# Kernel optimization log

Hardware: AMD Instinct MI355X
Metric: run time of the kernel (lower is better)

## Reference

```python
import jax, jax.numpy as jnp
import numpy as np

FACTOR = 1.0   # module's self.factor
EPS = 1e-6     # rmsnorm eps


def setup_inputs() -> dict:
    key = jax.random.key(0)
    k0, k1, k2, k3 = jax.random.split(key, 4)
    B, S = 4, 2048
    D_IN = D_STATE = D_OUT = 2048
    N_HEADS = 32
    HD = D_STATE // N_HEADS  # 64
    x = jax.random.normal(k0, (B, S, D_IN), jnp.float32)
    w_in = jax.random.normal(k1, (D_STATE, D_IN), jnp.float32) * 0.02
    b_in = jnp.zeros((D_STATE,), jnp.float32)
    state_weight = jax.random.normal(k2, (N_HEADS, HD, HD), jnp.float32) * 0.02
    norm_weight = jnp.ones((D_STATE,), jnp.float32)
    w_out = jax.random.normal(k3, (D_OUT, D_STATE), jnp.float32) * (0.02 / np.sqrt(2 * 24))
    return dict(x=x, w_in=w_in, b_in=b_in, state_weight=state_weight,
                norm_weight=norm_weight, w_out=w_out)


def _rnn_scan(xt, W):
    # xt: (B, S, N, H); W: (N, H, H)
    B, S, N, H = xt.shape

    def step(s, x_t):
        # s: (B, N, H) ; per-head linear recurrence with tanh nonlinearity
        s = jnp.tanh(jnp.einsum('bnh,nhk->bnk', s, W) + x_t)
        return s, s

    s0 = jnp.zeros((B, N, H), xt.dtype)
    _, states = jax.lax.scan(step, s0, jnp.swapaxes(xt, 0, 1))  # (S, B, N, H)
    return jnp.swapaxes(states, 0, 1)  # (B, S, N, H)


def reference(x, w_in, b_in, state_weight, norm_weight, w_out):
    B, S, _ = x.shape
    N, H, _ = state_weight.shape
    h = x @ w_in.T + b_in                      # input_projection: (B,S,state)
    h = h.reshape(B, S, N, H) * FACTOR
    W = state_weight * FACTOR
    states = _rnn_scan(h, W)                   # (B,S,N,H)
    y = states.reshape(B, S, N * H)
    # rmsnorm
    y = y * jax.lax.rsqrt(jnp.mean(y * y, axis=-1, keepdims=True) + EPS) * norm_weight
    return y @ w_out.T                         # output_projection (no bias)
```

## Files before the change

kernel.cpp:

```cpp
#include <hip/hip_runtime.h>
#include <hip/hip_bf16.h>
#include <cstdint>


typedef short bf16x8 __attribute__((ext_vector_type(8)));
typedef float f32x4 __attribute__((ext_vector_type(4)));
typedef _Float16 f16x2 __attribute__((ext_vector_type(2)));

#define GLD16(gp, lp)                                                          \
  __builtin_amdgcn_global_load_lds(                                            \
      (const __attribute__((address_space(1))) void*)(gp),                     \
      (__attribute__((address_space(3))) void*)(lp), 16, 0, 0)

__global__ __launch_bounds__(256) void cvt_f32_bf16(
    const float* __restrict__ in, __hip_bfloat16* __restrict__ out, int n4) {
  int i = blockIdx.x * 256 + threadIdx.x;
  if (i >= n4) return;
  float4 v = ((const float4*)in)[i];
  __hip_bfloat16 a = __float2bfloat16(v.x);
  __hip_bfloat16 b = __float2bfloat16(v.y);
  __hip_bfloat16 c = __float2bfloat16(v.z);
  __hip_bfloat16 d = __float2bfloat16(v.w);
  ushort4 p;
  p.x = *(unsigned short*)&a; p.y = *(unsigned short*)&b;
  p.z = *(unsigned short*)&c; p.w = *(unsigned short*)&d;
  ((ushort4*)out)[i] = p;
}

__global__ __launch_bounds__(512) void gemm_nt(
    const __hip_bfloat16* __restrict__ A, const __hip_bfloat16* __restrict__ B,
    const float* __restrict__ bias, float* __restrict__ C,
    int M, int N, int K) {
  __shared__ __hip_bfloat16 As[2][256 * 32];
  __shared__ __hip_bfloat16 Bs[2][256 * 32];
  const int tid  = threadIdx.x;
  const int lane = tid & 63;
  const int wave = tid >> 6;
  const int wm = wave >> 2;
  const int wn = wave & 3;

  const int id = blockIdx.y * gridDim.x + blockIdx.x;
  const int v = (id & 7) * 32 + (id >> 3);
  const long bm = (long)(v >> 3) * 256;
  const long bn = (long)(v & 7) * 256;

  const int r0 = tid >> 2;
  const int k0 = (tid & 3) * 8;
  const __hip_bfloat16* gA0 = A + (bm + r0) * (long)K + k0;
  const __hip_bfloat16* gA1 = A + (bm + 128 + r0) * (long)K + k0;
  const __hip_bfloat16* gB0 = B + (bn + r0) * (long)K + k0;
  const __hip_bfloat16* gB1 = B + (bn + 128 + r0) * (long)K + k0;

#define STAGE(sbuf, kt)                                                        \
  do {                                                                         \
    GLD16(gA0 + (kt) * 32, &As[sbuf][wave * 512]);                             \
    GLD16(gA1 + (kt) * 32, &As[sbuf][4096 + wave * 512]);                      \
    GLD16(gB0 + (kt) * 32, &Bs[sbuf][wave * 512]);                             \
    GLD16(gB1 + (kt) * 32, &Bs[sbuf][4096 + wave * 512]);                      \
  } while (0)

  const int fr = lane & 15;
  const int fk = (lane >> 4) * 8;

  f32x4 acc[8][4];
#pragma unroll
  for (int i = 0; i < 8; i++)
#pragma unroll
    for (int j = 0; j < 4; j++) acc[i][j] = {0.f, 0.f, 0.f, 0.f};

  STAGE(0, 0);

  const int nk = K >> 5;
  for (int kt = 0; kt < nk; kt++) {
    const int cur = kt & 1;
    if (kt + 1 < nk) {
      STAGE(cur ^ 1, kt + 1);
      asm volatile("s_waitcnt vmcnt(4)" ::: "memory");
    } else {
      asm volatile("s_waitcnt vmcnt(0)" ::: "memory");
    }
    __builtin_amdgcn_s_barrier();
    __builtin_amdgcn_sched_barrier(0);
    bf16x8 af[8], bfr[4];
#pragma unroll
    for (int t = 0; t < 8; t++)
      af[t] = *(const bf16x8*)&As[cur][(wm * 128 + t * 16 + fr) * 32 + fk];
#pragma unroll
    for (int t = 0; t < 4; t++)
      bfr[t] = *(const bf16x8*)&Bs[cur][(wn * 64 + t * 16 + fr) * 32 + fk];
    __builtin_amdgcn_s_setprio(1);
#pragma unroll
    for (int i = 0; i < 8; i++)
#pragma unroll
      for (int j = 0; j < 4; j++)
        acc[i][j] = __builtin_amdgcn_mfma_f32_16x16x32_bf16(
            af[i], bfr[j], acc[i][j], 0, 0, 0);
    __builtin_amdgcn_s_setprio(0);
    __builtin_amdgcn_sched_barrier(0);
    __builtin_amdgcn_s_barrier();
  }
#undef STAGE

  const int cr = (lane >> 4) * 4;
  const int cc = lane & 15;
#pragma unroll
  for (int j = 0; j < 4; j++) {
    const long n = bn + wn * 64 + j * 16 + cc;
    const float bv = bias ? bias[n] : 0.0f;
#pragma unroll
    for (int i = 0; i < 8; i++) {
      const long m = bm + wm * 128 + i * 16 + cr;
#pragma unroll
      for (int r = 0; r < 4; r++)
        C[(m + r) * (long)N + n] = acc[i][j][r] + bv;
    }
  }
}

__device__ __forceinline__ float tanh_fast(float z) {
  float e = __builtin_amdgcn_exp2f(z * 2.8853900817779268f);
  return 1.0f - 2.0f * __builtin_amdgcn_rcpf(e + 1.0f);
}

__global__ __launch_bounds__(64) void scan_kernel(
    const float* __restrict__ Wst, float* __restrict__ h) {
  const int b = blockIdx.x >> 5;
  const int n = blockIdx.x & 31;
  const int lane = threadIdx.x;
  const float* Wn = Wst + n * 4096;

  f16x2 w2[32];
#pragma unroll
  for (int p = 0; p < 32; p++) {
    f16x2 t;
    t.x = (_Float16)Wn[(2 * p) * 64 + lane];
    t.y = (_Float16)Wn[(2 * p + 1) * 64 + lane];
    w2[p] = t;
  }

  __shared__ alignas(16) unsigned short s_h[64];

  int4 sv[8];
#pragma unroll
  for (int q = 0; q < 8; q++) sv[q] = make_int4(0, 0, 0, 0);

  float* hp = h + ((size_t)b * 2048) * 2048 + n * 64 + lane;
  float xcur[8], xnxt[8];
#pragma unroll
  for (int i = 0; i < 8; i++) xcur[i] = hp[(size_t)i * 2048];

  const f16x2 z2 = {(_Float16)0.f, (_Float16)0.f};

  for (int t0 = 0; t0 < 2048; t0 += 8) {
    if (t0 + 8 < 2048) {
#pragma unroll
      for (int i = 0; i < 8; i++)
        xnxt[i] = hp[(size_t)(t0 + 8 + i) * 2048];
    }
#pragma unroll
    for (int i = 0; i < 8; i++) {
      f16x2 ac0 = z2, ac1 = z2, ac2 = z2, ac3 = z2;
#pragma unroll
      for (int q = 0; q < 8; q++) {
        ac0 = __builtin_elementwise_fma(__builtin_bit_cast(f16x2, sv[q].x),
                                        w2[4 * q + 0], ac0);
        ac1 = __builtin_elementwise_fma(__builtin_bit_cast(f16x2, sv[q].y),
                                        w2[4 * q + 1], ac1);
        ac2 = __builtin_elementwise_fma(__builtin_bit_cast(f16x2, sv[q].z),
                                        w2[4 * q + 2], ac2);
        ac3 = __builtin_elementwise_fma(__builtin_bit_cast(f16x2, sv[q].w),
                                        w2[4 * q + 3], ac3);
      }
      f16x2 p01 = ac0 + ac1;
      f16x2 p23 = ac2 + ac3;
      f16x2 pt = p01 + p23;
      float z = (float)pt.x + (float)pt.y + xcur[i];
      float sn = tanh_fast(z);
      _Float16 sh = (_Float16)sn;
      s_h[lane] = __builtin_bit_cast(unsigned short, sh);
#pragma unroll
      for (int q = 0; q < 8; q++) sv[q] = ((const int4*)s_h)[q];
      hp[(size_t)(t0 + i) * 2048] = sn;
    }
#pragma unroll
    for (int i = 0; i < 8; i++) xcur[i] = xnxt[i];
  }
}

__global__ __launch_bounds__(256) void rmsnorm_to_bf16(
    const float* __restrict__ Y, const float* __restrict__ g,
    __hip_bfloat16* __restrict__ O) {
  const long row = blockIdx.x;
  const float* yr = Y + row * 2048;
  const int tid = threadIdx.x;
  float4 v0 = ((const float4*)yr)[tid * 2];
  float4 v1 = ((const float4*)yr)[tid * 2 + 1];
  float ss = v0.x * v0.x + v0.y * v0.y + v0.z * v0.z + v0.w * v0.w +
             v1.x * v1.x + v1.y * v1.y + v1.z * v1.z + v1.w * v1.w;
#pragma unroll
  for (int off = 32; off > 0; off >>= 1) ss += __shfl_down(ss, off);
  __shared__ float red[4];
  if ((tid & 63) == 0) red[tid >> 6] = ss;
  __syncthreads();
  float inv = rsqrtf((red[0] + red[1] + red[2] + red[3]) * (1.0f / 2048.0f)
                     + 1e-6f);
  float4 g0 = ((const float4*)(g + tid * 8))[0];
  float4 g1 = ((const float4*)(g + tid * 8))[1];
  float ov[8] = {v0.x * inv * g0.x, v0.y * inv * g0.y,
                 v0.z * inv * g0.z, v0.w * inv * g0.w,
                 v1.x * inv * g1.x, v1.y * inv * g1.y,
                 v1.z * inv * g1.z, v1.w * inv * g1.w};
  ushort4 p0, p1;
  __hip_bfloat16 t;
  t = __float2bfloat16(ov[0]); p0.x = *(unsigned short*)&t;
  t = __float2bfloat16(ov[1]); p0.y = *(unsigned short*)&t;
  t = __float2bfloat16(ov[2]); p0.z = *(unsigned short*)&t;
  t = __float2bfloat16(ov[3]); p0.w = *(unsigned short*)&t;
  t = __float2bfloat16(ov[4]); p1.x = *(unsigned short*)&t;
  t = __float2bfloat16(ov[5]); p1.y = *(unsigned short*)&t;
  t = __float2bfloat16(ov[6]); p1.z = *(unsigned short*)&t;
  t = __float2bfloat16(ov[7]); p1.w = *(unsigned short*)&t;
  ushort4* op = (ushort4*)(O + row * 2048 + tid * 8);
  op[0] = p0;
  op[1] = p1;
}

extern "C" void kernel_launch(void* const* d_in, const int* in_sizes, int n_in,
                              void* d_out, int out_size, void* d_ws,
                              size_t ws_size, hipStream_t stream) {
  const float* x     = (const float*)d_in[0];
  const float* w_in  = (const float*)d_in[1];
  const float* b_in  = (const float*)d_in[2];
  const float* w_st  = (const float*)d_in[3];
  const float* nw    = (const float*)d_in[4];
  const float* w_out = (const float*)d_in[5];
  float* out = (float*)d_out;

  char* ws = (char*)d_ws;
  __hip_bfloat16* x_bf  = (__hip_bfloat16*)(ws);
  __hip_bfloat16* wi_bf = (__hip_bfloat16*)(ws + 33554432);
  __hip_bfloat16* wo_bf = (__hip_bfloat16*)(ws + 41943040);
  float* h              = (float*)(ws + 50331648);

  cvt_f32_bf16<<<16384, 256, 0, stream>>>(x, x_bf, 4194304);
  cvt_f32_bf16<<<4096, 256, 0, stream>>>(w_in, wi_bf, 1048576);
  cvt_f32_bf16<<<4096, 256, 0, stream>>>(w_out, wo_bf, 1048576);

  gemm_nt<<<dim3(8, 32), 512, 0, stream>>>(x_bf, wi_bf, b_in, h,
                                           8192, 2048, 2048);
  scan_kernel<<<128, 64, 0, stream>>>(w_st, h);
  rmsnorm_to_bf16<<<8192, 256, 0, stream>>>(h, nw, x_bf);
  gemm_nt<<<dim3(8, 32), 512, 0, stream>>>(x_bf, wo_bf, nullptr, out,
                                           8192, 2048, 2048);
}
```

Baseline: 710.4 us.

## Double K-tile depth to 64 with XOR-swizzled LDS layout in GEMM

Raises the GEMM K step from 32 to 64 per iteration, halving the number of barrier-synchronised loop trips and issuing twice as many MFMAs between barriers. LDS rows are now 64 bf16 wide, with an XOR swizzle on the 16-byte column chunk to avoid bank conflicts on fragment reads. This doubles LDS use to 128 KB per block and raises register pressure from the doubled fragments. The launch bound of two blocks per CU may not be reachable with that much shared memory.

```diff
diff --git a/kernel.cpp b/kernel.cpp
--- a/kernel.cpp
+++ b/kernel.cpp
@@ -27,12 +27,12 @@
   ((ushort4*)out)[i] = p;
 }
 
-__global__ __launch_bounds__(512) void gemm_nt(
+__global__ __launch_bounds__(512, 2) void gemm_nt(
     const __hip_bfloat16* __restrict__ A, const __hip_bfloat16* __restrict__ B,
     const float* __restrict__ bias, float* __restrict__ C,
     int M, int N, int K) {
-  __shared__ __hip_bfloat16 As[2][256 * 32];
-  __shared__ __hip_bfloat16 Bs[2][256 * 32];
+  __shared__ __hip_bfloat16 As[2][256 * 64];
+  __shared__ __hip_bfloat16 Bs[2][256 * 64];
   const int tid  = threadIdx.x;
   const int lane = tid & 63;
   const int wave = tid >> 6;
@@ -44,23 +44,30 @@
   const long bm = (long)(v >> 3) * 256;
   const long bn = (long)(v & 7) * 256;
 
-  const int r0 = tid >> 2;
-  const int k0 = (tid & 3) * 8;
-  const __hip_bfloat16* gA0 = A + (bm + r0) * (long)K + k0;
-  const __hip_bfloat16* gA1 = A + (bm + 128 + r0) * (long)K + k0;
-  const __hip_bfloat16* gB0 = B + (bn + r0) * (long)K + k0;
-  const __hip_bfloat16* gB1 = B + (bn + 128 + r0) * (long)K + k0;
+  const int srow = (wave << 3) + (lane >> 3);
+  const int scol = (((lane & 7) ^ ((lane >> 3) & 7)) << 3);
+  const __hip_bfloat16* gA = A + (bm + srow) * (long)K + scol;
+  const __hip_bfloat16* gB = B + (bn + srow) * (long)K + scol;
+  const long rstep = 64 * (long)K;
 
 #define STAGE(sbuf, kt)                                                        \
   do {                                                                         \
-    GLD16(gA0 + (kt) * 32, &As[sbuf][wave * 512]);                             \
-    GLD16(gA1 + (kt) * 32, &As[sbuf][4096 + wave * 512]);                      \
-    GLD16(gB0 + (kt) * 32, &Bs[sbuf][wave * 512]);                             \
-    GLD16(gB1 + (kt) * 32, &Bs[sbuf][4096 + wave * 512]);                      \
+    const long ko_ = (long)(kt) * 64;                                          \
+    GLD16(gA + ko_,             &As[sbuf][wave * 512]);                        \
+    GLD16(gA + ko_ + rstep,     &As[sbuf][4096 + wave * 512]);                 \
+    GLD16(gA + ko_ + 2 * rstep, &As[sbuf][8192 + wave * 512]);                 \
+    GLD16(gA + ko_ + 3 * rstep, &As[sbuf][12288 + wave * 512]);                \
+    GLD16(gB + ko_,             &Bs[sbuf][wave * 512]);                        \
+    GLD16(gB + ko_ + rstep,     &Bs[sbuf][4096 + wave * 512]);                 \
+    GLD16(gB + ko_ + 2 * rstep, &Bs[sbuf][8192 + wave * 512]);                 \
+    GLD16(gB + ko_ + 3 * rstep, &Bs[sbuf][12288 + wave * 512]);                \
   } while (0)
 
-  const int fr = lane & 15;
-  const int fk = (lane >> 4) * 8;
+  const int fr  = lane & 15;
+  const int fk8 = (lane >> 4) * 8;
+  const int xr  = (fr & 7) << 3;
+  const int ac0 = fk8 ^ xr;
+  const int ac1 = (32 + fk8) ^ xr;
 
   f32x4 acc[8][4];
 #pragma unroll
@@ -69,32 +76,43 @@
     for (int j = 0; j < 4; j++) acc[i][j] = {0.f, 0.f, 0.f, 0.f};
 
   STAGE(0, 0);
-
-  const int nk = K >> 5;
+  asm volatile("s_waitcnt vmcnt(0)" ::: "memory");
+  __builtin_amdgcn_s_barrier();
+
+  const int nk = K >> 6;
   for (int kt = 0; kt < nk; kt++) {
     const int cur = kt & 1;
     if (kt + 1 < nk) {
       STAGE(cur ^ 1, kt + 1);
-      asm volatile("s_waitcnt vmcnt(4)" ::: "memory");
+      asm volatile("s_waitcnt vmcnt(8)" ::: "memory");
     } else {
       asm volatile("s_waitcnt vmcnt(0)" ::: "memory");
     }
     __builtin_amdgcn_s_barrier();
     __builtin_amdgcn_sched_barrier(0);
-    bf16x8 af[8], bfr[4];
-#pragma unroll
-    for (int t = 0; t < 8; t++)
-      af[t] = *(const bf16x8*)&As[cur][(wm * 128 + t * 16 + fr) * 32 + fk];
-#pragma unroll
-    for (int t = 0; t < 4; t++)
-      bfr[t] = *(const bf16x8*)&Bs[cur][(wn * 64 + t * 16 + fr) * 32 + fk];
+    bf16x8 af[8][2], bfr[4][2];
+#pragma unroll
+    for (int t = 0; t < 8; t++) {
+      const int rb = (wm * 128 + t * 16 + fr) * 64;
+      af[t][0] = *(const bf16x8*)&As[cur][rb + ac0];
+      af[t][1] = *(const bf16x8*)&As[cur][rb + ac1];
+    }
+#pragma unroll
+    for (int j = 0; j < 4; j++) {
+      const int rb = (wn * 64 + j * 16 + fr) * 64;
+      bfr[j][0] = *(const bf16x8*)&Bs[cur][rb + ac0];
+      bfr[j][1] = *(const bf16x8*)&Bs[cur][rb + ac1];
+    }
     __builtin_amdgcn_s_setprio(1);
 #pragma unroll
     for (int i = 0; i < 8; i++)
 #pragma unroll
-      for (int j = 0; j < 4; j++)
+      for (int j = 0; j < 4; j++) {
         acc[i][j] = __builtin_amdgcn_mfma_f32_16x16x32_bf16(
-            af[i], bfr[j], acc[i][j], 0, 0, 0);
+            af[i][0], bfr[j][0], acc[i][j], 0, 0, 0);
+        acc[i][j] = __builtin_amdgcn_mfma_f32_16x16x32_bf16(
+            af[i][1], bfr[j][1], acc[i][j], 0, 0, 0);
+      }
     __builtin_amdgcn_s_setprio(0);
     __builtin_amdgcn_sched_barrier(0);
     __builtin_amdgcn_s_barrier();
```

Measured after the change: 682.4 us. -3.9%, faster.
